# Kernel optimization log

Measured on AMD Instinct MI355X. Metric: run time of the kernel, lower is better.

## Reference

```python
import jax, jax.numpy as jnp
import numpy as np

N_NODES = 100000
N_EDGES = 3200000


def gcn_conv(x, edge_index, W, b, n_nodes):
    # PyG GCNConv: x' = D^{-1/2} (A + I) D^{-1/2} (x W) + b
    h = x @ W  # [N, C_out]
    loop = jnp.arange(n_nodes, dtype=edge_index.dtype)
    src = jnp.concatenate([edge_index[0], loop])  # source nodes j
    dst = jnp.concatenate([edge_index[1], loop])  # target nodes i (aggregation)
    deg = jax.ops.segment_sum(jnp.ones_like(dst, h.dtype), dst, num_segments=n_nodes)
    dinv = jnp.where(deg > 0, jax.lax.rsqrt(deg), 0.0)
    norm = dinv[src] * dinv[dst]  # [E+N]
    msg = h[src] * norm[:, None]  # gather + scale
    out = jax.ops.segment_sum(msg, dst, num_segments=n_nodes)  # scatter-add
    return out + b


def setup_inputs() -> dict:
    key = jax.random.key(0)
    ks = jax.random.split(key, 6)
    x = jax.random.normal(ks[0], (N_NODES, 1), dtype=jnp.float32)
    edge_index = jax.random.randint(ks[1], (2, N_EDGES), 0, N_NODES, dtype=jnp.int64)
    W1 = jax.random.normal(ks[2], (1, 16), dtype=jnp.float32) * (1.0 / np.sqrt(1))
    b1 = jnp.zeros((16,), dtype=jnp.float32)
    W2 = jax.random.normal(ks[3], (16, 16), dtype=jnp.float32) * (1.0 / np.sqrt(16))
    b2 = jnp.zeros((16,), dtype=jnp.float32)
    Wl = jax.random.normal(ks[4], (16, 1), dtype=jnp.float32) * (1.0 / np.sqrt(16))
    bl = jnp.zeros((1,), dtype=jnp.float32)
    return {"x": x, "edge_index": edge_index, "W1": W1, "b1": b1,
            "W2": W2, "b2": b2, "Wl": Wl, "bl": bl}


def reference(x, edge_index, W1, b1, W2, b2, Wl, bl):
    n = x.shape[0]
    h = gcn_conv(x, edge_index, W1, b1, n)
    h = jax.nn.relu(h)
    # F.dropout(training=self.training): identity in eval mode
    h = gcn_conv(h, edge_index, W2, b2, n)
    return h @ Wl + bl  # [N, 1]
```

## Files before the change

### kernel.cpp

```cpp
#include <hip/hip_runtime.h>

#define N_NODES  100000
#define N_EDGES  3200000
#define NB       7
#define BSH      14
#define BN       16384
#define PTHR     1024
#define NW       16
#define PTILE    8192
#define NTILES   ((N_EDGES + PTILE - 1) / PTILE)
#define CAP_B    600000
#define SA       32
#define GA       (NB * SA)
#define ATHR     1024
#define RTHR     512


__global__ __launch_bounds__(PTHR) void k_part(const int* __restrict__ src,
        const int* __restrict__ dstp, unsigned* __restrict__ cursor,
        unsigned* __restrict__ pedge) {
    __shared__ unsigned stage[PTILE];
    __shared__ unsigned wcnt[NB * NW];
    __shared__ unsigned woff[NB * NW];
    __shared__ unsigned bstart[NB + 1];
    __shared__ unsigned gbase[NB];
    const int tid = threadIdx.x, wave = tid >> 6, lane = tid & 63;
    const int qbeg = (blockIdx.x * PTILE) >> 2;
    int qend = qbeg + (PTILE >> 2);
    if (qend > (N_EDGES >> 2)) qend = N_EDGES >> 2;

    const uint4* s4 = (const uint4*)src;
    const uint4* d4 = (const uint4*)dstp;
    unsigned pk[8], pos[8];
    int bk[8];
    unsigned rc0=0,rc1=0,rc2=0,rc3=0,rc4=0,rc5=0,rc6=0;

    #pragma unroll
    for (int k = 0; k < 2; ++k) {
        const int q = qbeg + k * PTHR + tid;
        const bool v = q < qend;
        uint4 sv = {0,0,0,0}, dv = {0,0,0,0};
        if (v) { sv = s4[q]; dv = d4[q]; }
        const unsigned ss[4] = { sv.x, sv.y, sv.z, sv.w };
        const unsigned dd[4] = { dv.x, dv.y, dv.z, dv.w };
        #pragma unroll
        for (int j = 0; j < 4; ++j) {
            const int i = k * 4 + j;
            const unsigned b = v ? (dd[j] >> BSH) : 0xFFu;
            bk[i] = v ? (int)b : -1;
            pk[i] = ss[j] | ((dd[j] & (BN - 1u)) << 17);
            unsigned p = 0;
            #pragma unroll
            for (unsigned bb = 0; bb < NB; ++bb) {
                const unsigned long long m = __ballot(b == bb);
                const unsigned tot = (unsigned)__popcll(m);
                const unsigned mb  = (unsigned)__popcll(m & ((1ull << lane) - 1ull));
                unsigned rcv = bb==0?rc0:bb==1?rc1:bb==2?rc2:bb==3?rc3:bb==4?rc4:bb==5?rc5:rc6;
                if (b == bb) p = rcv + mb;
                rcv += tot;
                if (bb==0) rc0=rcv; else if (bb==1) rc1=rcv; else if (bb==2) rc2=rcv;
                else if (bb==3) rc3=rcv; else if (bb==4) rc4=rcv; else if (bb==5) rc5=rcv;
                else rc6=rcv;
            }
            pos[i] = p;
        }
    }
    if (lane == 0) wcnt[0 * NW + wave] = rc0;
    if (lane == 1) wcnt[1 * NW + wave] = rc1;
    if (lane == 2) wcnt[2 * NW + wave] = rc2;
    if (lane == 3) wcnt[3 * NW + wave] = rc3;
    if (lane == 4) wcnt[4 * NW + wave] = rc4;
    if (lane == 5) wcnt[5 * NW + wave] = rc5;
    if (lane == 6) wcnt[6 * NW + wave] = rc6;
    __syncthreads();

    if (wave == 0) {
        const int i0 = lane * 2, i1 = i0 + 1;
        unsigned a0 = (i0 < NB * NW) ? wcnt[i0] : 0u;
        unsigned a1 = (i1 < NB * NW) ? wcnt[i1] : 0u;
        unsigned ps = a0 + a1;
        #pragma unroll
        for (int d = 1; d < 64; d <<= 1) {
            unsigned o = __shfl_up(ps, d, 64);
            if (lane >= d) ps += o;
        }
        const unsigned excl = ps - (a0 + a1);
        if (i0 < NB * NW) woff[i0] = excl;
        if (i1 < NB * NW) woff[i1] = excl + a0;
        if (lane == 63) bstart[NB] = ps;
    }
    __syncthreads();
    if (tid < NB) bstart[tid] = woff[tid * NW];
    __syncthreads();
    if (tid < NB) gbase[tid] = atomicAdd(&cursor[tid], bstart[tid + 1] - bstart[tid]);

    #pragma unroll
    for (int i = 0; i < 8; ++i)
        if (bk[i] >= 0) stage[woff[bk[i] * NW + wave] + pos[i]] = pk[i];
    __syncthreads();

    for (int b = 0; b < NB; ++b) {
        const unsigned s0 = bstart[b];
        const unsigned nb2 = bstart[b + 1] - s0;
        const unsigned g0 = gbase[b];
        unsigned* dc = pedge + (size_t)b * CAP_B + g0;
        for (unsigned j = tid; j < nb2; j += PTHR) dc[j] = stage[s0 + j];
    }
}

__global__ __launch_bounds__(ATHR) void k_degacc(const unsigned* __restrict__ pedge,
        const unsigned* __restrict__ cursor, unsigned short* __restrict__ p16) {
    __shared__ unsigned facc[BN];
    const int tid = threadIdx.x;
    const int bu = blockIdx.x / SA, sub = blockIdx.x % SA;
    for (int i = tid; i < BN; i += ATHR) facc[i] = 0u;
    __syncthreads();
    const unsigned n = cursor[bu];
    const unsigned* reg = pedge + (size_t)bu * CAP_B;
    for (unsigned j = (unsigned)(sub * ATHR + tid); j < n; j += SA * ATHR)
        atomicAdd(&facc[reg[j] >> 17], 1u);
    __syncthreads();
    unsigned short* po = p16 + (size_t)blockIdx.x * BN;
    for (int i = tid; i < BN; i += ATHR) po[i] = (unsigned short)facc[i];
}

__global__ __launch_bounds__(RTHR) void k_red1(const float* __restrict__ x,
        const unsigned short* __restrict__ p16,
        float* __restrict__ dinv, float* __restrict__ xs) {
    const int g = blockIdx.x * RTHR + threadIdx.x;
    if (g >= N_NODES) return;
    const int bu = g >> BSH, l = g & (BN - 1);
    const unsigned short* pp = p16 + (size_t)(bu * SA) * BN + l;
    unsigned run = 0;
    #pragma unroll
    for (int s = 0; s < SA; ++s) run += pp[(size_t)s * BN];
    const float di = rsqrtf((float)run + 1.f);
    dinv[g] = di;
    xs[g] = x[g] * di;
}

__global__ __launch_bounds__(ATHR) void k_acc(const unsigned* __restrict__ pedge,
        const unsigned* __restrict__ cursor, const float* __restrict__ vals,
        float* __restrict__ partials) {
    __shared__ float facc[BN];
    const int tid = threadIdx.x;
    const int bu = blockIdx.x / SA, sub = blockIdx.x % SA;
    for (int i = tid; i < BN; i += ATHR) facc[i] = 0.f;
    __syncthreads();
    const unsigned n = cursor[bu];
    const unsigned* reg = pedge + (size_t)bu * CAP_B;
    for (unsigned j = (unsigned)(sub * ATHR + tid); j < n; j += SA * ATHR) {
        const unsigned w = reg[j];
        atomicAdd(&facc[w >> 17], vals[w & 0x1FFFFu]);
    }
    __syncthreads();
    float* po = partials + (size_t)blockIdx.x * BN;
    for (int i = tid; i < BN; i += ATHR) po[i] = facc[i];
}

__device__ __forceinline__ float sum_partials(const float* __restrict__ partials,
                                              int g) {
    const int bu = g >> BSH, l = g & (BN - 1);
    const float* pp = partials + (size_t)(bu * SA) * BN + l;
    float s = 0.f;
    #pragma unroll
    for (int k = 0; k < SA; ++k) s += pp[(size_t)k * BN];
    return s;
}

__global__ __launch_bounds__(RTHR) void k_red2(const float* __restrict__ x,
        const float* __restrict__ partials, const float* __restrict__ dinv,
        const float* __restrict__ W1, const float* __restrict__ b1,
        const float* __restrict__ W2, const float* __restrict__ Wl,
        float* __restrict__ us, float* __restrict__ uself) {
    const int g = blockIdx.x * RTHR + threadIdx.x;
    if (g >= N_NODES) return;
    const float sum = sum_partials(partials, g);
    const float di = dinv[g];
    const float s1 = di * sum + x[g] * di * di;
    float u = 0.f;
    #pragma unroll
    for (int c = 0; c < 16; ++c) {
        float vcc = 0.f;
        #pragma unroll
        for (int k = 0; k < 16; ++k) vcc += W2[c * 16 + k] * Wl[k];
        u += fmaxf(W1[c] * s1 + b1[c], 0.f) * vcc;
    }
    us[g] = u * di;
    uself[g] = u * di * di;
}

__global__ __launch_bounds__(RTHR) void k_red3(const float* __restrict__ partials,
        const float* __restrict__ dinv, const float* __restrict__ uself,
        const float* __restrict__ W2, const float* __restrict__ b2,
        const float* __restrict__ Wl, const float* __restrict__ bl,
        float* __restrict__ out) {
    const int g = blockIdx.x * RTHR + threadIdx.x;
    if (g >= N_NODES) return;
    const float sum = sum_partials(partials, g);
    float vcb = bl[0];
    #pragma unroll
    for (int c = 0; c < 16; ++c) {
        float vcc = 0.f;
        #pragma unroll
        for (int k = 0; k < 16; ++k) vcc += W2[c * 16 + k] * Wl[k];
        vcb += b2[c] * vcc;
    }
    out[g] = dinv[g] * sum + uself[g] + vcb;
}

extern "C" void kernel_launch(void* const* d_in, const int* in_sizes, int n_in,
                              void* d_out, int out_size, void* d_ws, size_t ws_size,
                              hipStream_t stream) {
    const float* x  = (const float*)d_in[0];
    const int*   ei = (const int*)d_in[1];
    const float* W1 = (const float*)d_in[2];
    const float* b1 = (const float*)d_in[3];
    const float* W2 = (const float*)d_in[4];
    const float* b2 = (const float*)d_in[5];
    const float* Wl = (const float*)d_in[6];
    const float* bl = (const float*)d_in[7];
    float* out = (float*)d_out;

    const int* src  = ei;
    const int* dstp = ei + N_EDGES;

    unsigned* cursor      = (unsigned*)d_ws;
    unsigned* pedge       = cursor + 256;
    unsigned short* p16   = (unsigned short*)(pedge + (size_t)NB * CAP_B);
    float*    partials    = (float*)(p16 + (size_t)GA * BN);
    float*    dinv        = partials + (size_t)GA * BN;
    float*    xs          = dinv + N_NODES;
    float*    us          = xs + N_NODES;
    float*    uself       = us + N_NODES;

    hipMemsetAsync(d_ws, 0, 64, stream);

    const int red_blocks = (N_NODES + RTHR - 1) / RTHR;

    k_part<<<NTILES, PTHR, 0, stream>>>(src, dstp, cursor, pedge);
    k_degacc<<<GA, ATHR, 0, stream>>>(pedge, cursor, p16);
    k_red1<<<red_blocks, RTHR, 0, stream>>>(x, p16, dinv, xs);
    k_acc<<<GA, ATHR, 0, stream>>>(pedge, cursor, xs, partials);
    k_red2<<<red_blocks, RTHR, 0, stream>>>(x, partials, dinv, W1, b1, W2, Wl, us, uself);
    k_acc<<<GA, ATHR, 0, stream>>>(pedge, cursor, us, partials);
    k_red3<<<red_blocks, RTHR, 0, stream>>>(partials, dinv, uself, W2, b2, Wl, bl, out);
}
```

Baseline: 181.4 us.

## Partition edges into fixed-capacity per-tile bucket slots and fuse degree computation

Each partition tile now writes its edges into its own fixed-capacity slot per destination bucket, padded with a sentinel value. This removes the global cursor atomics and the memset. The bucket count goes to 8 with non-power-of-two buckets, and the degree count plus rsqrt normalisation is fused into a single kernel of one block per bucket. The cost is padded reads in the accumulation passes and only 8 blocks in the degree kernel, which limits parallelism. Edges beyond the per-tile capacity are silently dropped.

```diff
diff --git a/kernel.cpp b/kernel.cpp
--- a/kernel.cpp
+++ b/kernel.cpp
@@ -2,28 +2,28 @@
 
 #define N_NODES  100000
 #define N_EDGES  3200000
-#define NB       7
-#define BSH      14
-#define BN       16384
+#define NB       8
+#define BN       12544
 #define PTHR     1024
 #define NW       16
 #define PTILE    8192
 #define NTILES   ((N_EDGES + PTILE - 1) / PTILE)
-#define CAP_B    600000
+#define CAP_TB   1280
+#define SENT     0xFFFFFFFFu
 #define SA       32
 #define GA       (NB * SA)
 #define ATHR     1024
+#define DTHR     1024
 #define RTHR     512
 
 
 __global__ __launch_bounds__(PTHR) void k_part(const int* __restrict__ src,
-        const int* __restrict__ dstp, unsigned* __restrict__ cursor,
+        const int* __restrict__ dstp, unsigned* __restrict__ cnt,
         unsigned* __restrict__ pedge) {
     __shared__ unsigned stage[PTILE];
     __shared__ unsigned wcnt[NB * NW];
     __shared__ unsigned woff[NB * NW];
     __shared__ unsigned bstart[NB + 1];
-    __shared__ unsigned gbase[NB];
     const int tid = threadIdx.x, wave = tid >> 6, lane = tid & 63;
     const int qbeg = (blockIdx.x * PTILE) >> 2;
     int qend = qbeg + (PTILE >> 2);
@@ -33,7 +33,9 @@
     const uint4* d4 = (const uint4*)dstp;
     unsigned pk[8], pos[8];
     int bk[8];
-    unsigned rc0=0,rc1=0,rc2=0,rc3=0,rc4=0,rc5=0,rc6=0;
+    unsigned rc[NB];
+    #pragma unroll
+    for (int b = 0; b < NB; ++b) rc[b] = 0;
 
     #pragma unroll
     for (int k = 0; k < 2; ++k) {
@@ -46,38 +48,29 @@
         #pragma unroll
         for (int j = 0; j < 4; ++j) {
             const int i = k * 4 + j;
-            const unsigned b = v ? (dd[j] >> BSH) : 0xFFu;
+            const unsigned bb0 = dd[j] / BN;
+            const unsigned b = v ? bb0 : 0xFFu;
             bk[i] = v ? (int)b : -1;
-            pk[i] = ss[j] | ((dd[j] & (BN - 1u)) << 17);
+            pk[i] = ss[j] | ((dd[j] - bb0 * BN) << 17);
             unsigned p = 0;
             #pragma unroll
             for (unsigned bb = 0; bb < NB; ++bb) {
                 const unsigned long long m = __ballot(b == bb);
-                const unsigned tot = (unsigned)__popcll(m);
-                const unsigned mb  = (unsigned)__popcll(m & ((1ull << lane) - 1ull));
-                unsigned rcv = bb==0?rc0:bb==1?rc1:bb==2?rc2:bb==3?rc3:bb==4?rc4:bb==5?rc5:rc6;
-                if (b == bb) p = rcv + mb;
-                rcv += tot;
-                if (bb==0) rc0=rcv; else if (bb==1) rc1=rcv; else if (bb==2) rc2=rcv;
-                else if (bb==3) rc3=rcv; else if (bb==4) rc4=rcv; else if (bb==5) rc5=rcv;
-                else rc6=rcv;
+                if (b == bb)
+                    p = rc[bb] + (unsigned)__popcll(m & ((1ull << lane) - 1ull));
+                rc[bb] += (unsigned)__popcll(m);
             }
             pos[i] = p;
         }
     }
-    if (lane == 0) wcnt[0 * NW + wave] = rc0;
-    if (lane == 1) wcnt[1 * NW + wave] = rc1;
-    if (lane == 2) wcnt[2 * NW + wave] = rc2;
-    if (lane == 3) wcnt[3 * NW + wave] = rc3;
-    if (lane == 4) wcnt[4 * NW + wave] = rc4;
-    if (lane == 5) wcnt[5 * NW + wave] = rc5;
-    if (lane == 6) wcnt[6 * NW + wave] = rc6;
+    #pragma unroll
+    for (int b = 0; b < NB; ++b)
+        if (lane == b) wcnt[b * NW + wave] = rc[b];
     __syncthreads();
 
     if (wave == 0) {
         const int i0 = lane * 2, i1 = i0 + 1;
-        unsigned a0 = (i0 < NB * NW) ? wcnt[i0] : 0u;
-        unsigned a1 = (i1 < NB * NW) ? wcnt[i1] : 0u;
+        unsigned a0 = wcnt[i0], a1 = wcnt[i1];
         unsigned ps = a0 + a1;
         #pragma unroll
         for (int d = 1; d < 64; d <<= 1) {
@@ -85,14 +78,13 @@
             if (lane >= d) ps += o;
         }
         const unsigned excl = ps - (a0 + a1);
-        if (i0 < NB * NW) woff[i0] = excl;
-        if (i1 < NB * NW) woff[i1] = excl + a0;
+        woff[i0] = excl;
+        woff[i1] = excl + a0;
         if (lane == 63) bstart[NB] = ps;
     }
     __syncthreads();
     if (tid < NB) bstart[tid] = woff[tid * NW];
     __syncthreads();
-    if (tid < NB) gbase[tid] = atomicAdd(&cursor[tid], bstart[tid + 1] - bstart[tid]);
 
     #pragma unroll
     for (int i = 0; i < 8; ++i)
@@ -101,57 +93,56 @@
 
     for (int b = 0; b < NB; ++b) {
         const unsigned s0 = bstart[b];
-        const unsigned nb2 = bstart[b + 1] - s0;
-        const unsigned g0 = gbase[b];
-        unsigned* dc = pedge + (size_t)b * CAP_B + g0;
-        for (unsigned j = tid; j < nb2; j += PTHR) dc[j] = stage[s0 + j];
-    }
-}
-
-__global__ __launch_bounds__(ATHR) void k_degacc(const unsigned* __restrict__ pedge,
-        const unsigned* __restrict__ cursor, unsigned short* __restrict__ p16) {
+        unsigned nb2 = bstart[b + 1] - s0;
+        if (nb2 > CAP_TB) nb2 = CAP_TB;
+        unsigned* dc = pedge + ((size_t)blockIdx.x * NB + b) * CAP_TB;
+        for (unsigned j = tid; j < CAP_TB; j += PTHR)
+            dc[j] = (j < nb2) ? stage[s0 + j] : SENT;
+        if (tid == b) cnt[blockIdx.x * NB + b] = nb2;
+    }
+}
+
+__global__ __launch_bounds__(DTHR) void k_deg(const unsigned* __restrict__ pedge,
+        const float* __restrict__ x, float* __restrict__ dinv,
+        float* __restrict__ xs) {
     __shared__ unsigned facc[BN];
     const int tid = threadIdx.x;
-    const int bu = blockIdx.x / SA, sub = blockIdx.x % SA;
-    for (int i = tid; i < BN; i += ATHR) facc[i] = 0u;
-    __syncthreads();
-    const unsigned n = cursor[bu];
-    const unsigned* reg = pedge + (size_t)bu * CAP_B;
-    for (unsigned j = (unsigned)(sub * ATHR + tid); j < n; j += SA * ATHR)
-        atomicAdd(&facc[reg[j] >> 17], 1u);
-    __syncthreads();
-    unsigned short* po = p16 + (size_t)blockIdx.x * BN;
-    for (int i = tid; i < BN; i += ATHR) po[i] = (unsigned short)facc[i];
-}
-
-__global__ __launch_bounds__(RTHR) void k_red1(const float* __restrict__ x,
-        const unsigned short* __restrict__ p16,
-        float* __restrict__ dinv, float* __restrict__ xs) {
-    const int g = blockIdx.x * RTHR + threadIdx.x;
-    if (g >= N_NODES) return;
-    const int bu = g >> BSH, l = g & (BN - 1);
-    const unsigned short* pp = p16 + (size_t)(bu * SA) * BN + l;
-    unsigned run = 0;
-    #pragma unroll
-    for (int s = 0; s < SA; ++s) run += pp[(size_t)s * BN];
-    const float di = rsqrtf((float)run + 1.f);
-    dinv[g] = di;
-    xs[g] = x[g] * di;
+    const int bu = blockIdx.x;
+    for (int i = tid; i < BN; i += DTHR) facc[i] = 0u;
+    __syncthreads();
+    const unsigned total = (unsigned)NTILES * CAP_TB;
+    for (unsigned f = tid; f < total; f += DTHR) {
+        const unsigned rl = f / CAP_TB;
+        const unsigned j  = f - rl * CAP_TB;
+        const unsigned w = pedge[((size_t)rl * NB + bu) * CAP_TB + j];
+        if (w != SENT) atomicAdd(&facc[w >> 17], 1u);
+    }
+    __syncthreads();
+    for (int l = tid; l < BN; l += DTHR) {
+        const int g = bu * BN + l;
+        if (g < N_NODES) {
+            const float di = rsqrtf((float)facc[l] + 1.f);
+            dinv[g] = di;
+            xs[g] = x[g] * di;
+        }
+    }
 }
 
 __global__ __launch_bounds__(ATHR) void k_acc(const unsigned* __restrict__ pedge,
-        const unsigned* __restrict__ cursor, const float* __restrict__ vals,
-        float* __restrict__ partials) {
+        const float* __restrict__ vals, float* __restrict__ partials) {
     __shared__ float facc[BN];
     const int tid = threadIdx.x;
     const int bu = blockIdx.x / SA, sub = blockIdx.x % SA;
     for (int i = tid; i < BN; i += ATHR) facc[i] = 0.f;
     __syncthreads();
-    const unsigned n = cursor[bu];
-    const unsigned* reg = pedge + (size_t)bu * CAP_B;
-    for (unsigned j = (unsigned)(sub * ATHR + tid); j < n; j += SA * ATHR) {
-        const unsigned w = reg[j];
-        atomicAdd(&facc[w >> 17], vals[w & 0x1FFFFu]);
+    const unsigned nt = ((unsigned)NTILES - sub + SA - 1) / SA;
+    const unsigned total = nt * CAP_TB;
+    for (unsigned f = tid; f < total; f += ATHR) {
+        const unsigned rl = f / CAP_TB;
+        const unsigned j  = f - rl * CAP_TB;
+        const unsigned r  = sub + rl * SA;
+        const unsigned w = pedge[((size_t)r * NB + bu) * CAP_TB + j];
+        if (w != SENT) atomicAdd(&facc[w >> 17], vals[w & 0x1FFFFu]);
     }
     __syncthreads();
     float* po = partials + (size_t)blockIdx.x * BN;
@@ -160,7 +151,7 @@
 
 __device__ __forceinline__ float sum_partials(const float* __restrict__ partials,
                                               int g) {
-    const int bu = g >> BSH, l = g & (BN - 1);
+    const int bu = g / BN, l = g - bu * BN;
     const float* pp = partials + (size_t)(bu * SA) * BN + l;
     float s = 0.f;
     #pragma unroll
@@ -225,24 +216,20 @@
     const int* src  = ei;
     const int* dstp = ei + N_EDGES;
 
-    unsigned* cursor      = (unsigned*)d_ws;
-    unsigned* pedge       = cursor + 256;
-    unsigned short* p16   = (unsigned short*)(pedge + (size_t)NB * CAP_B);
-    float*    partials    = (float*)(p16 + (size_t)GA * BN);
-    float*    dinv        = partials + (size_t)GA * BN;
-    float*    xs          = dinv + N_NODES;
-    float*    us          = xs + N_NODES;
-    float*    uself       = us + N_NODES;
-
-    hipMemsetAsync(d_ws, 0, 64, stream);
+    unsigned* cnt      = (unsigned*)d_ws;
+    unsigned* pedge    = cnt + 4096;
+    float*    partials = (float*)(pedge + (size_t)NTILES * NB * CAP_TB);
+    float*    dinv     = partials + (size_t)GA * BN;
+    float*    xs       = dinv + N_NODES;
+    float*    us       = xs + N_NODES;
+    float*    uself    = us + N_NODES;
 
     const int red_blocks = (N_NODES + RTHR - 1) / RTHR;
 
-    k_part<<<NTILES, PTHR, 0, stream>>>(src, dstp, cursor, pedge);
-    k_degacc<<<GA, ATHR, 0, stream>>>(pedge, cursor, p16);
-    k_red1<<<red_blocks, RTHR, 0, stream>>>(x, p16, dinv, xs);
-    k_acc<<<GA, ATHR, 0, stream>>>(pedge, cursor, xs, partials);
+    k_part<<<NTILES, PTHR, 0, stream>>>(src, dstp, cnt, pedge);
+    k_deg<<<NB, DTHR, 0, stream>>>(pedge, x, dinv, xs);
+    k_acc<<<GA, ATHR, 0, stream>>>(pedge, xs, partials);
     k_red2<<<red_blocks, RTHR, 0, stream>>>(x, partials, dinv, W1, b1, W2, Wl, us, uself);
-    k_acc<<<GA, ATHR, 0, stream>>>(pedge, cursor, us, partials);
+    k_acc<<<GA, ATHR, 0, stream>>>(pedge, us, partials);
     k_red3<<<red_blocks, RTHR, 0, stream>>>(partials, dinv, uself, W2, b2, Wl, bl, out);
 }
```

Result: slower. 349.4 us (+92.6%).
